# Kernel tuning notes

Hardware: AMD Instinct MI355X
Metric: run time of the kernel (lower is better)

The kernel has to match this reference:

```python
import jax, jax.numpy as jnp
import numpy as np

EPS = 1e-5

def _linear(x, w, b):
    # torch nn.Linear convention: w is [out, in]
    return jnp.einsum('...i,oi->...o', x, w) + b

def _l2_normalize(x, axis=-1):
    n = jnp.sqrt(jnp.sum(x * x, axis=axis, keepdims=True))
    return x / jnp.maximum(n, 1e-12)

def _online_softmax_scan(sim):
    # sim: [B, H, L]. Running max m_t and running sum s_t = sum_{i<=t} exp(sim_i - m_t)
    def combine(a, b):
        ma, sa = a
        mb, sb = b
        m = jnp.maximum(ma, mb)
        s = sa * jnp.exp(ma - m) + sb * jnp.exp(mb - m)
        return m, s
    m_scan, s_scan = jax.lax.associative_scan(combine, (sim, jnp.ones_like(sim)), axis=2)
    return m_scan, s_scan


def setup_inputs() -> dict:
    key = jax.random.key(0)
    ks = jax.random.split(key, 8)
    B, L, D = 2, 2048, 256
    H, h = 8, 32
    s = 1.0 / np.sqrt(D)
    inp = {
        'x': jax.random.normal(ks[0], (B, L, D), jnp.float32),
        'wq_w': jax.random.normal(ks[1], (D, D), jnp.float32) * s,
        'wq_b': jnp.zeros((D,), jnp.float32),
        'wk_w': jax.random.normal(ks[2], (D, D), jnp.float32) * s,
        'wk_b': jnp.zeros((D,), jnp.float32),
        'wv_w': jax.random.normal(ks[3], (D, D), jnp.float32) * s,
        'wv_b': jnp.zeros((D,), jnp.float32),
        'wo_w': jax.random.normal(ks[4], (D, D), jnp.float32) * s,
        'wo_b': jnp.zeros((D,), jnp.float32),
        'wg_w': jax.random.normal(ks[5], (1, h * h), jnp.float32) * (1.0 / np.sqrt(h * h)),
        'wg_b': jnp.zeros((1,), jnp.float32),
        'kv_norm_scale': jnp.ones((1, H, 1, h, h), jnp.float32),
        'qk_norm_scale': jnp.full((1, H, 1), 1.0 / np.sqrt(h), jnp.float32),
    }
    return inp


def reference(x, wq_w, wq_b, wk_w, wk_b, wv_w, wv_b, wo_w, wo_b,
              wg_w, wg_b, kv_norm_scale, qk_norm_scale):
    B, L, D = x.shape
    H, h = kv_norm_scale.shape[1], kv_norm_scale.shape[3]

    q = _linear(x, wq_w, wq_b).reshape(B, L, H, h).transpose(0, 2, 1, 3)  # bhld
    k = _linear(x, wk_w, wk_b).reshape(B, L, H, h).transpose(0, 2, 1, 3)
    v = _linear(x, wv_w, wv_b).reshape(B, L, H, h).transpose(0, 2, 1, 3)

    sim = jnp.einsum('bhld,bhld->bhl', q, k) * qk_norm_scale  # [B,H,L]

    k = _l2_normalize(k)
    v = _l2_normalize(v)

    # outer-product KV state per position: [B,H,L,h,h]
    Z = jnp.einsum('bhld,bhle->bhlde', v, k) * kv_norm_scale

    # gating: squared ReLU of linear over flattened h*h features
    gate_inputs = Z.reshape(B, H, L, h * h)
    gates_logits = jnp.einsum('bhli,oi->bhlo', gate_inputs, wg_w) + wg_b  # [B,H,L,1]
    gates = jnp.square(jax.nn.relu(gates_logits)) + EPS
    gates = gates[..., None]  # [B,H,L,1,1]
    gated_Z = gates * Z

    # associative scans along L
    m_scan, s_scan = _online_softmax_scan(sim)        # [B,H,L]
    Z_scan = jnp.cumsum(gated_Z, axis=2)              # [B,H,L,h,h]
    g_scan = jnp.cumsum(gates, axis=2)                # [B,H,L,1,1]

    softmax_weights = (jnp.exp(sim - m_scan) / (s_scan + EPS))[..., None, None]
    gated_weights = Z_scan / (g_scan + EPS)
    attn_weights = gated_weights * (1.0 + jax.nn.silu(softmax_weights))

    ctxt = jnp.einsum('bhld,bhlde->bhle', q, attn_weights)
    ctxt = ctxt.transpose(0, 2, 1, 3).reshape(B, L, D)
    return _linear(ctxt, wo_w, wo_b)
```

## Files before the change

### kernel.cpp

```cpp
#include <hip/hip_runtime.h>
#include <math.h>

#define EPSV 1e-5f

static constexpr int Ls = 2048, Hh = 8;
static constexpr int NCH = 64, T = 32;

typedef unsigned short u16;
using frag  = __attribute__((ext_vector_type(8))) short;
using f32x4 = __attribute__((ext_vector_type(4))) float;

__device__ __forceinline__ void split_bf16(float v, u16& hi, u16& lo) {
    const unsigned u = __float_as_uint(v);
    hi = (u16)(u >> 16);
    const float hf = __uint_as_float((unsigned)hi << 16);
    lo = (u16)(__float_as_uint(v - hf) >> 16);
}

__device__ __forceinline__ unsigned pk2(u16 a, u16 b) {
    return (unsigned)a | ((unsigned)b << 16);
}

__device__ __forceinline__ void split8(const float4& a, const float4& b,
                                       uint4& hi, uint4& lo) {
    u16 h[8], l[8];
    const float f[8] = {a.x, a.y, a.z, a.w, b.x, b.y, b.z, b.w};
#pragma unroll
    for (int i = 0; i < 8; ++i) split_bf16(f[i], h[i], l[i]);
    hi = make_uint4(pk2(h[0], h[1]), pk2(h[2], h[3]), pk2(h[4], h[5]), pk2(h[6], h[7]));
    lo = make_uint4(pk2(l[0], l[1]), pk2(l[2], l[3]), pk2(l[4], l[5]), pk2(l[6], l[7]));
}

__global__ __launch_bounds__(256) void qkv_fused(
    const float* __restrict__ x,
    const float* __restrict__ wq, const float* __restrict__ wk, const float* __restrict__ wv,
    const float* __restrict__ bq, const float* __restrict__ bk, const float* __restrict__ bv,
    const float* __restrict__ wg_w, const float* __restrict__ wg_b,
    const float* __restrict__ kvs, const float* __restrict__ qks,
    float* __restrict__ qh, float* __restrict__ kh, float* __restrict__ vh,
    float* __restrict__ simG, float* __restrict__ gG,
    float* __restrict__ ZcT, float* __restrict__ mT, float* __restrict__ sT,
    float* __restrict__ gTt)
{
    constexpr int LDK = 40;
    constexpr int LDT = 68;
    __shared__ __align__(16) float smemf[3 * 64 * LDT];
    __shared__ __align__(16) float wkT[2][32 * 36];
    __shared__ float lsim[2][64], lg2[2][64];

    u16* As_hi = (u16*)smemf;
    u16* As_lo = As_hi + 2560;
    u16* Wst   = As_lo + 2560;
    float* Qt = smemf;
    float* Kt = Qt + 64 * LDT;
    float* Vt = Kt + 64 * LDT;

    const int tid = threadIdx.x;
    const int mt = blockIdx.x, nt = blockIdx.y;
    const int m0 = mt * 64, ncol0 = nt * 64;
    const int bidx = m0 >> 11, lg = m0 & (Ls - 1);
    const int wave = tid >> 6, lane = tid & 63;
    const int l15 = lane & 15, quad = lane >> 4;
    const int srow = tid >> 2, sk = (tid & 3) * 8;

    for (int i = tid; i < 2048; i += 256) {
        const int h = i >> 10, de = i & 1023;
        const int d = de >> 5, e = de & 31;
        wkT[h][e * 36 + d] = wg_w[de] * kvs[(nt * 2 + h) * 1024 + de];
    }

    const float* Wsrc[3] = {wq, wk, wv};
    f32x4 acc[3][4] = {};

    for (int k0 = 0; k0 < 256; k0 += 32) {
        const float4 a0 = *(const float4*)&x[(size_t)(m0 + srow) * 256 + k0 + sk];
        const float4 a1 = *(const float4*)&x[(size_t)(m0 + srow) * 256 + k0 + sk + 4];
        float4 w0[3], w1[3];
#pragma unroll
        for (int w = 0; w < 3; ++w) {
            w0[w] = *(const float4*)&Wsrc[w][(size_t)(ncol0 + srow) * 256 + k0 + sk];
            w1[w] = *(const float4*)&Wsrc[w][(size_t)(ncol0 + srow) * 256 + k0 + sk + 4];
        }
        __syncthreads();
        {
            uint4 hi, lo;
            split8(a0, a1, hi, lo);
            *(uint4*)&As_hi[srow * LDK + sk] = hi;
            *(uint4*)&As_lo[srow * LDK + sk] = lo;
#pragma unroll
            for (int w = 0; w < 3; ++w) {
                split8(w0[w], w1[w], hi, lo);
                *(uint4*)&Wst[w * 5120 + srow * LDK + sk] = hi;
                *(uint4*)&Wst[w * 5120 + 2560 + srow * LDK + sk] = lo;
            }
        }
        __syncthreads();

        const frag ah = *(const frag*)&As_hi[(wave * 16 + l15) * LDK + quad * 8];
        const frag al = *(const frag*)&As_lo[(wave * 16 + l15) * LDK + quad * 8];
#pragma unroll
        for (int w = 0; w < 3; ++w)
#pragma unroll
            for (int cf = 0; cf < 4; ++cf) {
                const u16* bp = &Wst[w * 5120 + (cf * 16 + l15) * LDK + quad * 8];
                const frag bh = *(const frag*)bp;
                const frag bl = *(const frag*)(bp + 2560);
                acc[w][cf] = __builtin_amdgcn_mfma_f32_16x16x32_bf16(ah, bh, acc[w][cf], 0, 0, 0);
                acc[w][cf] = __builtin_amdgcn_mfma_f32_16x16x32_bf16(ah, bl, acc[w][cf], 0, 0, 0);
                acc[w][cf] = __builtin_amdgcn_mfma_f32_16x16x32_bf16(al, bh, acc[w][cf], 0, 0, 0);
            }
    }
    __syncthreads();

    {
        float* tiles[3] = {Qt, Kt, Vt};
        const float* biases[3] = {bq, bk, bv};
#pragma unroll
        for (int w = 0; w < 3; ++w)
#pragma unroll
            for (int cf = 0; cf < 4; ++cf) {
                const int col = cf * 16 + l15;
                const float bias = biases[w][ncol0 + col];
#pragma unroll
                for (int r = 0; r < 4; ++r) {
                    const int m = wave * 16 + quad * 4 + r;
                    tiles[w][m * LDT + col] = acc[w][cf][r] + bias;
                }
            }
    }
    __syncthreads();

    if (tid < 128) {
        const int h = tid >> 6, l = tid & 63;
        const int rb = l * LDT + h * 32;
        float4 kr[8], vr[8];
        float ksum = 0.f, vsum = 0.f, qk = 0.f;
#pragma unroll
        for (int e4 = 0; e4 < 8; ++e4) {
            kr[e4] = *(const float4*)&Kt[rb + e4 * 4];
            vr[e4] = *(const float4*)&Vt[rb + e4 * 4];
            const float4 q4 = *(const float4*)&Qt[rb + e4 * 4];
            ksum += kr[e4].x * kr[e4].x + kr[e4].y * kr[e4].y + kr[e4].z * kr[e4].z + kr[e4].w * kr[e4].w;
            vsum += vr[e4].x * vr[e4].x + vr[e4].y * vr[e4].y + vr[e4].z * vr[e4].z + vr[e4].w * vr[e4].w;
            qk   += q4.x * kr[e4].x + q4.y * kr[e4].y + q4.z * kr[e4].z + q4.w * kr[e4].w;
        }
        const float kscale = 1.f / fmaxf(sqrtf(ksum), 1e-12f);
        const float vscale = 1.f / fmaxf(sqrtf(vsum), 1e-12f);
#pragma unroll
        for (int e4 = 0; e4 < 8; ++e4) {
            float4 k4 = kr[e4], v4 = vr[e4];
            k4.x *= kscale; k4.y *= kscale; k4.z *= kscale; k4.w *= kscale;
            v4.x *= vscale; v4.y *= vscale; v4.z *= vscale; v4.w *= vscale;
            *(float4*)&Kt[rb + e4 * 4] = k4;
            *(float4*)&Vt[rb + e4 * 4] = v4;
        }
        const float sim = qk * qks[nt * 2 + h];
        lsim[h][l] = sim;
        simG[(size_t)(bidx * 8 + nt * 2 + h) * Ls + lg + l] = sim;
    }
    __syncthreads();

    {
        const float* tl[3] = {Qt, Kt, Vt};
        float* gl[3] = {qh, kh, vh};
#pragma unroll
        for (int arr = 0; arr < 3; ++arr)
#pragma unroll
            for (int it = 0; it < 4; ++it) {
                const int idx = it * 1024 + tid * 4;
                const int h = idx >> 11, rem = idx & 2047;
                const int l = rem >> 5, e4 = rem & 31;
                const float4 v = *(const float4*)&tl[arr][l * LDT + h * 32 + e4];
                *(float4*)&gl[arr][(size_t)(bidx * 8 + nt * 2 + h) * 65536 +
                                   (size_t)(lg + l) * 32 + e4] = v;
            }
    }

    {
        const int task = tid >> 1, half = tid & 1;
        const int h = task >> 6, l = task & 63;
        float4 vr[8];
#pragma unroll
        for (int d4 = 0; d4 < 8; ++d4)
            vr[d4] = *(const float4*)&Vt[l * LDT + h * 32 + d4 * 4];
        float u = 0.f;
        const int e0 = half * 16;
#pragma unroll 4
        for (int e = e0; e < e0 + 16; ++e) {
            float4 s4 = make_float4(0.f, 0.f, 0.f, 0.f);
#pragma unroll
            for (int d4 = 0; d4 < 8; ++d4) {
                const float4 w4 = *(const float4*)&wkT[h][e * 36 + d4 * 4];
                s4.x = fmaf(vr[d4].x, w4.x, s4.x);
                s4.y = fmaf(vr[d4].y, w4.y, s4.y);
                s4.z = fmaf(vr[d4].z, w4.z, s4.z);
                s4.w = fmaf(vr[d4].w, w4.w, s4.w);
            }
            u = fmaf(s4.x + s4.y + s4.z + s4.w, Kt[l * LDT + h * 32 + e], u);
        }
        u += __shfl_xor(u, 1);
        if (half == 0) {
            const float r = fmaxf(u + wg_b[0], 0.f);
            const float g = r * r + EPSV;
            lg2[h][l] = g;
            gG[(size_t)(bidx * 8 + nt * 2 + h) * Ls + lg + l] = g;
        }
    }
    __syncthreads();

    {
        const int d = tid >> 3, e4m = (tid & 7) * 4;
#pragma unroll
        for (int h = 0; h < 2; ++h)
#pragma unroll
            for (int cc = 0; cc < 2; ++cc) {
                float4 z4 = make_float4(0.f, 0.f, 0.f, 0.f);
#pragma unroll 8
                for (int l = 0; l < 32; ++l) {
                    const int lr = cc * 32 + l;
                    const float gv = lg2[h][lr] * Vt[lr * LDT + h * 32 + d];
                    const float4 k4 = *(const float4*)&Kt[lr * LDT + h * 32 + e4m];
                    z4.x = fmaf(gv, k4.x, z4.x);
                    z4.y = fmaf(gv, k4.y, z4.y);
                    z4.z = fmaf(gv, k4.z, z4.z);
                    z4.w = fmaf(gv, k4.w, z4.w);
                }
                const int bhg = bidx * 8 + nt * 2 + h;
                const int cg = (lg >> 5) + cc;
                *(float4*)&ZcT[((size_t)bhg * NCH + cg) * 1024 + d * 32 + e4m] = z4;
            }
    }

    {
        const int h = wave >> 1, cc = wave & 1;
        if (lane < 32) {
            const int lr = cc * 32 + lane;
            float m = lsim[h][lr], s = 1.f, g = lg2[h][lr];
#pragma unroll
            for (int off = 16; off; off >>= 1) {
                const float mo = __shfl_xor(m, off);
                const float so = __shfl_xor(s, off);
                const float mn = fmaxf(m, mo);
                s = s * __expf(m - mn) + so * __expf(mo - mn);
                m = mn;
                g += __shfl_xor(g, off);
            }
            if (lane == 0) {
                const int bhg = bidx * 8 + nt * 2 + h;
                const int cg = (lg >> 5) + cc;
                mT[bhg * NCH + cg] = m;
                sT[bhg * NCH + cg] = s;
                gTt[bhg * NCH + cg] = g;
            }
        }
    }
}

__global__ __launch_bounds__(256) void prefix_kernel(
    float* __restrict__ Zc, float* __restrict__ mT, float* __restrict__ sT,
    float* __restrict__ gTt,
    const float* __restrict__ kvs, float* __restrict__ aW, float* __restrict__ bW,
    int* __restrict__ flagW)
{
    __shared__ float sc[64 * 64];
    const int bh = blockIdx.x, seg = blockIdx.y;
    const int tid = threadIdx.x;
    float* Zb = Zc + (size_t)bh * NCH * 1024 + seg * 64;

#pragma unroll
    for (int it = 0; it < 16; ++it) {
        const int idx = it * 256 + tid;
        const int cc = idx >> 6, e = idx & 63;
        sc[idx] = Zb[(size_t)cc * 1024 + e];
    }
    __syncthreads();
#pragma unroll
    for (int st = 1; st < 64; st <<= 1) {
        float tmp[16];
#pragma unroll
        for (int it = 0; it < 16; ++it) {
            const int idx = it * 256 + tid;
            tmp[it] = ((idx >> 6) >= st) ? sc[idx - st * 64] : 0.f;
        }
        __syncthreads();
#pragma unroll
        for (int it = 0; it < 16; ++it) sc[it * 256 + tid] += tmp[it];
        __syncthreads();
    }
#pragma unroll
    for (int it = 0; it < 16; ++it) {
        const int idx = it * 256 + tid;
        const int cc = idx >> 6, e = idx & 63;
        Zb[(size_t)cc * 1024 + e] = cc ? sc[idx - 64] : 0.f;
    }

    if (seg == 0 && tid < 64) {
        float m = mT[bh * NCH + tid], s = sT[bh * NCH + tid], g = gTt[bh * NCH + tid];
#pragma unroll
        for (int off = 1; off < 64; off <<= 1) {
            const float mo = __shfl_up(m, off);
            const float so = __shfl_up(s, off);
            const float go = __shfl_up(g, off);
            if (tid >= off) {
                const float mn = fmaxf(m, mo);
                s = s * __expf(m - mn) + so * __expf(mo - mn);
                m = mn;
                g += go;
            }
        }
        float me = __shfl_up(m, 1), se = __shfl_up(s, 1), ge = __shfl_up(g, 1);
        if (tid == 0) { me = -1e30f; se = 0.f; ge = 0.f; }
        mT[bh * NCH + tid] = me;
        sT[bh * NCH + tid] = se;
        gTt[bh * NCH + tid] = ge;
    }

    if (bh == 0 && seg == 1) {
        const int h = tid >> 5, e = tid & 31;
        const float* K = kvs + h * 1024;
        const float k00 = K[0];
        int ok = (k00 != 0.0f);
        for (int d = 0; d < 32; ++d) {
            const float lhs = K[d * 32 + e] * k00;
            const float rhs = K[d * 32] * K[e];
            const float diff = fabsf(lhs - rhs);
            if (diff > 1e-6f * fmaxf(fmaxf(fabsf(lhs), fabsf(rhs)), 1e-20f)) ok = 0;
        }
        aW[h * 32 + e] = K[e * 32];
        bW[h * 32 + e] = (k00 != 0.0f) ? K[e] / k00 : 0.f;
        const int allok = __syncthreads_and(ok);
        if (tid == 0) flagW[0] = allok;
    }
}

__global__ __launch_bounds__(256) void chunk_out_kernel(
    const float* __restrict__ qh, const float* __restrict__ knG, const float* __restrict__ vnG,
    const float* __restrict__ simG, const float* __restrict__ gG,
    const float* __restrict__ kvs,
    const float* __restrict__ ZcP, const float* __restrict__ mP,
    const float* __restrict__ sP, const float* __restrict__ gP,
    const float* __restrict__ aW, const float* __restrict__ bW,
    const int* __restrict__ flagW,
    u16* __restrict__ chi, u16* __restrict__ clo)
{
    __shared__ __align__(16) float qa[1024], knb[1024], zp[1024], sW[1024];
    __shared__ __align__(16) float vnT[32 * 36];
    __shared__ float lkvs[1024];
    __shared__ float lgS[32], lsimS[32], lwgt[32];
    const int tid = threadIdx.x;
    const int c = blockIdx.x, bh = blockIdx.y, h = bh & 7, b = bh >> 3;
    const int l = tid >> 3, e4 = (tid & 7) * 4;
    const size_t base4 = ((size_t)bh * Ls + (size_t)c * T) * 8 + tid;
    const int flag = flagW[0];

    const float4 qv4 = ((const float4*)qh)[base4];
    const float4 kn4 = ((const float4*)knG)[base4];
    const float4 vn4 = ((const float4*)vnG)[base4];
    const float4 z4  = ((const float4*)ZcP)[((size_t)bh * NCH + c) * 256 + tid];
    const float4 la4 = *(const float4*)&aW[h * 32 + e4];
    const float4 lb4 = *(const float4*)&bW[h * 32 + e4];
    if (tid < 32) {
        lgS[tid] = gG[bh * Ls + c * T + tid];
        lsimS[tid] = simG[bh * Ls + c * T + tid];
    }
    if (!flag) {
        *(float4*)&lkvs[tid * 4] = *(const float4*)&kvs[h * 1024 + tid * 4];
    }
    {
        float4 q = qv4, k = kn4;
        if (flag) {
            q.x *= la4.x; q.y *= la4.y; q.z *= la4.z; q.w *= la4.w;
            k.x *= lb4.x; k.y *= lb4.y; k.z *= lb4.z; k.w *= lb4.w;
        }
        *(float4*)&qa[l * 32 + e4] = q;
        *(float4*)&knb[l * 32 + e4] = k;
        *(float4*)&zp[tid * 4] = z4;
        vnT[(e4 + 0) * 36 + l] = vn4.x;
        vnT[(e4 + 1) * 36 + l] = vn4.y;
        vnT[(e4 + 2) * 36 + l] = vn4.z;
        vnT[(e4 + 3) * 36 + l] = vn4.w;
    }
    __syncthreads();

    if (tid < 32) {
        float m = lsimS[tid], s = 1.f, g = lgS[tid];
#pragma unroll
        for (int off = 1; off < 32; off <<= 1) {
            const float mo = __shfl_up(m, off);
            const float so = __shfl_up(s, off);
            const float go = __shfl_up(g, off);
            if (tid >= off) {
                const float mn = fmaxf(m, mo);
                s = s * __expf(m - mn) + so * __expf(mo - mn);
                m = mn;
                g += go;
            }
        }
        const float mp = mP[bh * NCH + c];
        const float sp = sP[bh * NCH + c];
        const float gp = gP[bh * NCH + c];
        const float mn = fmaxf(mp, m);
        s = sp * __expf(mp - mn) + s * __expf(m - mn);
        m = mn;
        g += gp;
        const float sw = __expf(lsimS[tid] - m) / (s + EPSV);
        const float sig = 1.f / (1.f + __expf(-sw));
        lwgt[tid] = (1.f + sw * sig) / (g + EPSV);
    }

    float4 y4 = make_float4(0.f, 0.f, 0.f, 0.f);
    if (flag) {
        float qrow[32];
#pragma unroll
        for (int d4 = 0; d4 < 8; ++d4)
            *(float4*)&qrow[d4 * 4] = *(const float4*)&qa[l * 32 + d4 * 4];
        float4 s4 = make_float4(0.f, 0.f, 0.f, 0.f);
#pragma unroll 8
        for (int d = 0; d < 32; ++d) {
            const float qd = qrow[d];
            const float4 v4 = *(const float4*)&vnT[d * 36 + e4];
            const float4 p4 = *(const float4*)&zp[d * 32 + e4];
            s4.x = fmaf(qd, v4.x, s4.x);
            s4.y = fmaf(qd, v4.y, s4.y);
            s4.z = fmaf(qd, v4.z, s4.z);
            s4.w = fmaf(qd, v4.w, s4.w);
            y4.x = fmaf(qd, p4.x, y4.x);
            y4.y = fmaf(qd, p4.y, y4.y);
            y4.z = fmaf(qd, p4.z, y4.z);
            y4.w = fmaf(qd, p4.w, y4.w);
        }
        y4.x *= lb4.x; y4.y *= lb4.y; y4.z *= lb4.z; y4.w *= lb4.w;
        const float4 lg4 = *(const float4*)&lgS[e4];
        float4 sm;
        sm.x = (e4 + 0 <= l) ? lg4.x * s4.x : 0.f;
        sm.y = (e4 + 1 <= l) ? lg4.y * s4.y : 0.f;
        sm.z = (e4 + 2 <= l) ? lg4.z * s4.z : 0.f;
        sm.w = (e4 + 3 <= l) ? lg4.w * s4.w : 0.f;
        *(float4*)&sW[l * 32 + e4] = sm;
        __syncthreads();
        float srow[32];
#pragma unroll
        for (int j4 = 0; j4 < 8; ++j4)
            *(float4*)&srow[j4 * 4] = *(const float4*)&sW[l * 32 + j4 * 4];
#pragma unroll 8
        for (int j = 0; j < 32; ++j) {
            const float sj = srow[j];
            const float4 k4 = *(const float4*)&knb[j * 32 + e4];
            y4.x = fmaf(sj, k4.x, y4.x);
            y4.y = fmaf(sj, k4.y, y4.y);
            y4.z = fmaf(sj, k4.z, y4.z);
            y4.w = fmaf(sj, k4.w, y4.w);
        }
    } else {
        __syncthreads();
        float* yp = &y4.x;
#pragma unroll
        for (int i = 0; i < 4; ++i) {
            const int e = e4 + i;
            float qe[32];
#pragma unroll
            for (int d = 0; d < 32; ++d)
                qe[d] = qa[l * 32 + d] * lkvs[d * 32 + e];
            float y = 0.f;
#pragma unroll
            for (int d = 0; d < 32; ++d)
                y = fmaf(qe[d], zp[d * 32 + e], y);
            for (int j = 0; j < 32; ++j) {
                float s = 0.f;
#pragma unroll
                for (int d = 0; d < 32; ++d)
                    s = fmaf(qe[d], vnT[d * 36 + j], s);
                if (j <= l) y = fmaf(lgS[j] * s, knb[j * 32 + e], y);
            }
            yp[i] = y;
        }
    }
    const float w = lwgt[l];
    ushort4 hi4, lo4;
    split_bf16(y4.x * w, hi4.x, lo4.x);
    split_bf16(y4.y * w, hi4.y, lo4.y);
    split_bf16(y4.z * w, hi4.z, lo4.z);
    split_bf16(y4.w * w, hi4.w, lo4.w);
    const size_t oidx = ((size_t)(b * Ls + c * T + l)) * 256 + h * 32 + e4;
    *(ushort4*)&chi[oidx] = hi4;
    *(ushort4*)&clo[oidx] = lo4;
}

__global__ __launch_bounds__(256) void out_gemm(
    const u16* __restrict__ Ahi, const u16* __restrict__ Alo,
    const float* __restrict__ wo, const float* __restrict__ bo,
    float* __restrict__ out)
{
    constexpr int LDK = 40;
    __shared__ __align__(16) u16 As_hi[64 * LDK];
    __shared__ __align__(16) u16 As_lo[64 * LDK];
    __shared__ __align__(16) u16 Ws_hi[64 * LDK];
    __shared__ __align__(16) u16 Ws_lo[64 * LDK];

    const int tid = threadIdx.x;
    const int mt = blockIdx.x, nt = blockIdx.y;
    const int m0 = mt * 64, ncol0 = nt * 64;
    const int wave = tid >> 6, lane = tid & 63;
    const int l15 = lane & 15, quad = lane >> 4;
    const int srow = tid >> 2, sk = (tid & 3) * 8;

    f32x4 acc[4] = {};

    for (int k0 = 0; k0 < 256; k0 += 32) {
        const uint4 ah = *(const uint4*)&Ahi[(size_t)(m0 + srow) * 256 + k0 + sk];
        const uint4 al = *(const uint4*)&Alo[(size_t)(m0 + srow) * 256 + k0 + sk];
        const float4 w0 = *(const float4*)&wo[(size_t)(ncol0 + srow) * 256 + k0 + sk];
        const float4 w1 = *(const float4*)&wo[(size_t)(ncol0 + srow) * 256 + k0 + sk + 4];
        __syncthreads();
        uint4 whi, wlo;
        split8(w0, w1, whi, wlo);
        *(uint4*)&As_hi[srow * LDK + sk] = ah;
        *(uint4*)&As_lo[srow * LDK + sk] = al;
        *(uint4*)&Ws_hi[srow * LDK + sk] = whi;
        *(uint4*)&Ws_lo[srow * LDK + sk] = wlo;
        __syncthreads();

        const frag fah = *(const frag*)&As_hi[(wave * 16 + l15) * LDK + quad * 8];
        const frag fal = *(const frag*)&As_lo[(wave * 16 + l15) * LDK + quad * 8];
#pragma unroll
        for (int cf = 0; cf < 4; ++cf) {
            const frag fbh = *(const frag*)&Ws_hi[(cf * 16 + l15) * LDK + quad * 8];
            const frag fbl = *(const frag*)&Ws_lo[(cf * 16 + l15) * LDK + quad * 8];
            acc[cf] = __builtin_amdgcn_mfma_f32_16x16x32_bf16(fah, fbh, acc[cf], 0, 0, 0);
            acc[cf] = __builtin_amdgcn_mfma_f32_16x16x32_bf16(fah, fbl, acc[cf], 0, 0, 0);
            acc[cf] = __builtin_amdgcn_mfma_f32_16x16x32_bf16(fal, fbh, acc[cf], 0, 0, 0);
        }
    }

#pragma unroll
    for (int cf = 0; cf < 4; ++cf) {
        const int o = ncol0 + cf * 16 + l15;
        const float bias = bo[o];
#pragma unroll
        for (int r = 0; r < 4; ++r) {
            const int rm = m0 + wave * 16 + quad * 4 + r;
            out[(size_t)rm * 256 + o] = acc[cf][r] + bias;
        }
    }
}

extern "C" void kernel_launch(void* const* d_in, const int* in_sizes, int n_in,
                              void* d_out, int out_size, void* d_ws, size_t ws_size,
                              hipStream_t stream) {
    const float* x    = (const float*)d_in[0];
    const float* wq_w = (const float*)d_in[1];
    const float* wq_b = (const float*)d_in[2];
    const float* wk_w = (const float*)d_in[3];
    const float* wk_b = (const float*)d_in[4];
    const float* wv_w = (const float*)d_in[5];
    const float* wv_b = (const float*)d_in[6];
    const float* wo_w = (const float*)d_in[7];
    const float* wo_b = (const float*)d_in[8];
    const float* wg_w = (const float*)d_in[9];
    const float* wg_b = (const float*)d_in[10];
    const float* kvs  = (const float*)d_in[11];
    const float* qks  = (const float*)d_in[12];
    float* out = (float*)d_out;

    u16* chi = (u16*)d_ws;
    u16* clo = chi + 1048576;
    float* qh   = (float*)(clo + 1048576);
    float* kh   = qh + 1048576;
    float* vh   = kh + 1048576;
    float* ZcT  = vh + 1048576;
    float* simG = ZcT + 1048576;
    float* gG   = simG + 32768;
    float* mT   = gG + 32768;
    float* sT   = mT + 1024;
    float* gTt  = sT + 1024;
    float* aW   = gTt + 1024;
    float* bW   = aW + 256;
    int* flagW  = (int*)(bW + 256);

    qkv_fused<<<dim3(64, 4), 256, 0, stream>>>(
        x, wq_w, wk_w, wv_w, wq_b, wk_b, wv_b, wg_w, wg_b, kvs, qks,
        qh, kh, vh, simG, gG, ZcT, mT, sT, gTt);
    prefix_kernel<<<dim3(16, 16), 256, 0, stream>>>(
        ZcT, mT, sT, gTt, kvs, aW, bW, flagW);
    chunk_out_kernel<<<dim3(NCH, 16), 256, 0, stream>>>(
        qh, kh, vh, simG, gG, kvs, ZcT, mT, sT, gTt, aW, bW, flagW, chi, clo);
    out_gemm<<<dim3(64, 4), 256, 0, stream>>>(
        chi, clo, wo_w, wo_b, out);
}
```

Measured before the change: 157.6 us.

## Merge four kernels into one cooperative persistent kernel with grid syncs

Folds the QKV projection, prefix scan, chunk output and output GEMM kernels into a single mega_kernel that is launched cooperatively with 256 blocks and separates phases with grid-wide syncs. If cooperative launch is unavailable or fails, it falls back to four per-phase launches. The goal is to remove the launch gaps between kernels. The phase-0 GEMM is also re-tiled so each wave owns 16 output columns and walks all four row tiles, reusing each B fragment. Risks: the middle phases have to be remapped onto 256 blocks, grid syncs cost time, and a register-heavy body may limit occupancy.

```diff
diff --git a/kernel.cpp b/kernel.cpp
--- a/kernel.cpp
+++ b/kernel.cpp
@@ -1,7 +1,10 @@
 #include <hip/hip_runtime.h>
+#include <hip/hip_cooperative_groups.h>
 #include <math.h>
 
 #define EPSV 1e-5f
+
+namespace cg = cooperative_groups;
 
 static constexpr int Ls = 2048, Hh = 8;
 static constexpr int NCH = 64, T = 32;
@@ -31,515 +34,518 @@
     lo = make_uint4(pk2(l[0], l[1]), pk2(l[2], l[3]), pk2(l[4], l[5]), pk2(l[6], l[7]));
 }
 
-__global__ __launch_bounds__(256) void qkv_fused(
-    const float* __restrict__ x,
-    const float* __restrict__ wq, const float* __restrict__ wk, const float* __restrict__ wv,
-    const float* __restrict__ bq, const float* __restrict__ bk, const float* __restrict__ bv,
-    const float* __restrict__ wg_w, const float* __restrict__ wg_b,
-    const float* __restrict__ kvs, const float* __restrict__ qks,
-    float* __restrict__ qh, float* __restrict__ kh, float* __restrict__ vh,
-    float* __restrict__ simG, float* __restrict__ gG,
-    float* __restrict__ ZcT, float* __restrict__ mT, float* __restrict__ sT,
-    float* __restrict__ gTt)
-{
-    constexpr int LDK = 40;
-    constexpr int LDT = 68;
-    __shared__ __align__(16) float smemf[3 * 64 * LDT];
-    __shared__ __align__(16) float wkT[2][32 * 36];
-    __shared__ float lsim[2][64], lg2[2][64];
-
-    u16* As_hi = (u16*)smemf;
-    u16* As_lo = As_hi + 2560;
-    u16* Wst   = As_lo + 2560;
-    float* Qt = smemf;
-    float* Kt = Qt + 64 * LDT;
-    float* Vt = Kt + 64 * LDT;
+struct Params {
+    const float *x, *wq, *wk, *wv, *bq, *bk, *bv, *wo, *bo, *wg_w, *wg_b, *kvs, *qks;
+    float *qh, *kh, *vh, *simG, *gG, *ZcT, *mT, *sT, *gTt, *aW, *bW;
+    int* flagW;
+    u16 *chi, *clo;
+    float* out;
+};
+
+__global__ __launch_bounds__(256) void mega_kernel(Params p, int phase) {
+    __shared__ __align__(16) float smem[15616];
 
     const int tid = threadIdx.x;
-    const int mt = blockIdx.x, nt = blockIdx.y;
-    const int m0 = mt * 64, ncol0 = nt * 64;
-    const int bidx = m0 >> 11, lg = m0 & (Ls - 1);
+    const int bid = blockIdx.x;
     const int wave = tid >> 6, lane = tid & 63;
     const int l15 = lane & 15, quad = lane >> 4;
-    const int srow = tid >> 2, sk = (tid & 3) * 8;
-
-    for (int i = tid; i < 2048; i += 256) {
-        const int h = i >> 10, de = i & 1023;
-        const int d = de >> 5, e = de & 31;
-        wkT[h][e * 36 + d] = wg_w[de] * kvs[(nt * 2 + h) * 1024 + de];
-    }
-
-    const float* Wsrc[3] = {wq, wk, wv};
-    f32x4 acc[3][4] = {};
-
-    for (int k0 = 0; k0 < 256; k0 += 32) {
-        const float4 a0 = *(const float4*)&x[(size_t)(m0 + srow) * 256 + k0 + sk];
-        const float4 a1 = *(const float4*)&x[(size_t)(m0 + srow) * 256 + k0 + sk + 4];
-        float4 w0[3], w1[3];
-#pragma unroll
-        for (int w = 0; w < 3; ++w) {
-            w0[w] = *(const float4*)&Wsrc[w][(size_t)(ncol0 + srow) * 256 + k0 + sk];
-            w1[w] = *(const float4*)&Wsrc[w][(size_t)(ncol0 + srow) * 256 + k0 + sk + 4];
-        }
-        __syncthreads();
-        {
-            uint4 hi, lo;
-            split8(a0, a1, hi, lo);
-            *(uint4*)&As_hi[srow * LDK + sk] = hi;
-            *(uint4*)&As_lo[srow * LDK + sk] = lo;
+
+    if (phase < 0 || phase == 0) {
+        constexpr int LDK = 40;
+        constexpr int LDT = 68;
+        u16* As_hi = (u16*)smem;
+        u16* As_lo = As_hi + 2560;
+        u16* Wst   = As_lo + 2560;
+        float* Qt = smem;
+        float* Kt = Qt + 64 * LDT;
+        float* Vt = Kt + 64 * LDT;
+        float* wkT  = smem + 13056;
+        float* lsim = smem + 15360;
+        float* lg2  = smem + 15488;
+
+        const int mt = bid & 63, nt = bid >> 6;
+        const int m0 = mt * 64, ncol0 = nt * 64;
+        const int bidx = m0 >> 11, lg = m0 & (Ls - 1);
+        const int srow = tid >> 2, sk = (tid & 3) * 8;
+
+        for (int i = tid; i < 2048; i += 256) {
+            const int h = i >> 10, de = i & 1023;
+            const int d = de >> 5, e = de & 31;
+            wkT[h * 1152 + e * 36 + d] = p.wg_w[de] * p.kvs[(nt * 2 + h) * 1024 + de];
+        }
+
+        const float* Wsrc[3] = {p.wq, p.wk, p.wv};
+        f32x4 acc[3][4] = {};
+
+        for (int k0 = 0; k0 < 256; k0 += 32) {
+            const float4 a0 = *(const float4*)&p.x[(size_t)(m0 + srow) * 256 + k0 + sk];
+            const float4 a1 = *(const float4*)&p.x[(size_t)(m0 + srow) * 256 + k0 + sk + 4];
+            float4 w0[3], w1[3];
 #pragma unroll
             for (int w = 0; w < 3; ++w) {
-                split8(w0[w], w1[w], hi, lo);
-                *(uint4*)&Wst[w * 5120 + srow * LDK + sk] = hi;
-                *(uint4*)&Wst[w * 5120 + 2560 + srow * LDK + sk] = lo;
-            }
-        }
-        __syncthreads();
-
-        const frag ah = *(const frag*)&As_hi[(wave * 16 + l15) * LDK + quad * 8];
-        const frag al = *(const frag*)&As_lo[(wave * 16 + l15) * LDK + quad * 8];
-#pragma unroll
-        for (int w = 0; w < 3; ++w)
-#pragma unroll
-            for (int cf = 0; cf < 4; ++cf) {
-                const u16* bp = &Wst[w * 5120 + (cf * 16 + l15) * LDK + quad * 8];
+                w0[w] = *(const float4*)&Wsrc[w][(size_t)(ncol0 + srow) * 256 + k0 + sk];
+                w1[w] = *(const float4*)&Wsrc[w][(size_t)(ncol0 + srow) * 256 + k0 + sk + 4];
+            }
+            __syncthreads();
+            {
+                uint4 hi, lo;
+                split8(a0, a1, hi, lo);
+                *(uint4*)&As_hi[srow * LDK + sk] = hi;
+                *(uint4*)&As_lo[srow * LDK + sk] = lo;
+#pragma unroll
+                for (int w = 0; w < 3; ++w) {
+                    split8(w0[w], w1[w], hi, lo);
+                    *(uint4*)&Wst[w * 5120 + srow * LDK + sk] = hi;
+                    *(uint4*)&Wst[w * 5120 + 2560 + srow * LDK + sk] = lo;
+                }
+            }
+            __syncthreads();
+
+            frag ah[4], al[4];
+#pragma unroll
+            for (int tm = 0; tm < 4; ++tm) {
+                const int r = tm * 16 + l15;
+                ah[tm] = *(const frag*)&As_hi[r * LDK + quad * 8];
+                al[tm] = *(const frag*)&As_lo[r * LDK + quad * 8];
+            }
+#pragma unroll
+            for (int w = 0; w < 3; ++w) {
+                const u16* bp = &Wst[w * 5120 + (wave * 16 + l15) * LDK + quad * 8];
                 const frag bh = *(const frag*)bp;
                 const frag bl = *(const frag*)(bp + 2560);
-                acc[w][cf] = __builtin_amdgcn_mfma_f32_16x16x32_bf16(ah, bh, acc[w][cf], 0, 0, 0);
-                acc[w][cf] = __builtin_amdgcn_mfma_f32_16x16x32_bf16(ah, bl, acc[w][cf], 0, 0, 0);
-                acc[w][cf] = __builtin_amdgcn_mfma_f32_16x16x32_bf16(al, bh, acc[w][cf], 0, 0, 0);
-            }
+#pragma unroll
+                for (int tm = 0; tm < 4; ++tm) {
+                    acc[w][tm] = __builtin_amdgcn_mfma_f32_16x16x32_bf16(ah[tm], bh, acc[w][tm], 0, 0, 0);
+                    acc[w][tm] = __builtin_amdgcn_mfma_f32_16x16x32_bf16(ah[tm], bl, acc[w][tm], 0, 0, 0);
+                    acc[w][tm] = __builtin_amdgcn_mfma_f32_16x16x32_bf16(al[tm], bh, acc[w][tm], 0, 0, 0);
+                }
+            }
+        }
+        __syncthreads();
+
+        {
+            float* tiles[3] = {Qt, Kt, Vt};
+            const float* biases[3] = {p.bq, p.bk, p.bv};
+#pragma unroll
+            for (int w = 0; w < 3; ++w) {
+                const int col = wave * 16 + l15;
+                const float bias = biases[w][ncol0 + col];
+#pragma unroll
+                for (int tm = 0; tm < 4; ++tm)
+#pragma unroll
+                    for (int r = 0; r < 4; ++r) {
+                        const int m = tm * 16 + quad * 4 + r;
+                        tiles[w][m * LDT + col] = acc[w][tm][r] + bias;
+                    }
+            }
+        }
+        __syncthreads();
+
+        if (tid < 128) {
+            const int h = tid >> 6, l = tid & 63;
+            const int rb = l * LDT + h * 32;
+            float4 kr[8], vr[8];
+            float ksum = 0.f, vsum = 0.f, qk = 0.f;
+#pragma unroll
+            for (int e4 = 0; e4 < 8; ++e4) {
+                kr[e4] = *(const float4*)&Kt[rb + e4 * 4];
+                vr[e4] = *(const float4*)&Vt[rb + e4 * 4];
+                const float4 q4 = *(const float4*)&Qt[rb + e4 * 4];
+                ksum += kr[e4].x * kr[e4].x + kr[e4].y * kr[e4].y + kr[e4].z * kr[e4].z + kr[e4].w * kr[e4].w;
+                vsum += vr[e4].x * vr[e4].x + vr[e4].y * vr[e4].y + vr[e4].z * vr[e4].z + vr[e4].w * vr[e4].w;
+                qk   += q4.x * kr[e4].x + q4.y * kr[e4].y + q4.z * kr[e4].z + q4.w * kr[e4].w;
+            }
+            const float kscale = 1.f / fmaxf(sqrtf(ksum), 1e-12f);
+            const float vscale = 1.f / fmaxf(sqrtf(vsum), 1e-12f);
+#pragma unroll
+            for (int e4 = 0; e4 < 8; ++e4) {
+                float4 k4 = kr[e4], v4 = vr[e4];
+                k4.x *= kscale; k4.y *= kscale; k4.z *= kscale; k4.w *= kscale;
+                v4.x *= vscale; v4.y *= vscale; v4.z *= vscale; v4.w *= vscale;
+                *(float4*)&Kt[rb + e4 * 4] = k4;
+                *(float4*)&Vt[rb + e4 * 4] = v4;
+            }
+            const float sim = qk * p.qks[nt * 2 + h];
+            lsim[h * 64 + l] = sim;
+            p.simG[(size_t)(bidx * 8 + nt * 2 + h) * Ls + lg + l] = sim;
+        }
+        __syncthreads();
+
+        {
+            const float* tl[3] = {Qt, Kt, Vt};
+            float* gl[3] = {p.qh, p.kh, p.vh};
+#pragma unroll
+            for (int arr = 0; arr < 3; ++arr)
+#pragma unroll
+                for (int it = 0; it < 4; ++it) {
+                    const int idx = it * 1024 + tid * 4;
+                    const int h = idx >> 11, rem = idx & 2047;
+                    const int l = rem >> 5, e4 = rem & 31;
+                    const float4 v = *(const float4*)&tl[arr][l * LDT + h * 32 + e4];
+                    *(float4*)&gl[arr][(size_t)(bidx * 8 + nt * 2 + h) * 65536 +
+                                       (size_t)(lg + l) * 32 + e4] = v;
+                }
+        }
+
+        {
+            const int task = tid >> 1, half = tid & 1;
+            const int h = task >> 6, l = task & 63;
+            float4 vr[8];
+#pragma unroll
+            for (int d4 = 0; d4 < 8; ++d4)
+                vr[d4] = *(const float4*)&Vt[l * LDT + h * 32 + d4 * 4];
+            float u = 0.f;
+            const int e0 = half * 16;
+#pragma unroll 4
+            for (int e = e0; e < e0 + 16; ++e) {
+                float4 s4 = make_float4(0.f, 0.f, 0.f, 0.f);
+#pragma unroll
+                for (int d4 = 0; d4 < 8; ++d4) {
+                    const float4 w4 = *(const float4*)&wkT[h * 1152 + e * 36 + d4 * 4];
+                    s4.x = fmaf(vr[d4].x, w4.x, s4.x);
+                    s4.y = fmaf(vr[d4].y, w4.y, s4.y);
+                    s4.z = fmaf(vr[d4].z, w4.z, s4.z);
+                    s4.w = fmaf(vr[d4].w, w4.w, s4.w);
+                }
+                u = fmaf(s4.x + s4.y + s4.z + s4.w, Kt[l * LDT + h * 32 + e], u);
+            }
+            u += __shfl_xor(u, 1);
+            if (half == 0) {
+                const float r = fmaxf(u + p.wg_b[0], 0.f);
+                const float g = r * r + EPSV;
+                lg2[h * 64 + l] = g;
+                p.gG[(size_t)(bidx * 8 + nt * 2 + h) * Ls + lg + l] = g;
+            }
+        }
+        __syncthreads();
+
+        {
+            const int d = tid >> 3, e4m = (tid & 7) * 4;
+#pragma unroll
+            for (int h = 0; h < 2; ++h)
+#pragma unroll
+                for (int cc = 0; cc < 2; ++cc) {
+                    float4 z4 = make_float4(0.f, 0.f, 0.f, 0.f);
+#pragma unroll 8
+                    for (int l = 0; l < 32; ++l) {
+                        const int lr = cc * 32 + l;
+                        const float gv = lg2[h * 64 + lr] * Vt[lr * LDT + h * 32 + d];
+                        const float4 k4 = *(const float4*)&Kt[lr * LDT + h * 32 + e4m];
+                        z4.x = fmaf(gv, k4.x, z4.x);
+                        z4.y = fmaf(gv, k4.y, z4.y);
+                        z4.z = fmaf(gv, k4.z, z4.z);
+                        z4.w = fmaf(gv, k4.w, z4.w);
+                    }
+                    const int bhg = bidx * 8 + nt * 2 + h;
+                    const int cg = (lg >> 5) + cc;
+                    *(float4*)&p.ZcT[((size_t)bhg * NCH + cg) * 1024 + d * 32 + e4m] = z4;
+                }
+        }
+
+        {
+            const int h = wave >> 1, cc = wave & 1;
+            if (lane < 32) {
+                const int lr = cc * 32 + lane;
+                float m = lsim[h * 64 + lr], s = 1.f, g = lg2[h * 64 + lr];
+#pragma unroll
+                for (int off = 16; off; off >>= 1) {
+                    const float mo = __shfl_xor(m, off);
+                    const float so = __shfl_xor(s, off);
+                    const float mn = fmaxf(m, mo);
+                    s = s * __expf(m - mn) + so * __expf(mo - mn);
+                    m = mn;
+                    g += __shfl_xor(g, off);
+                }
+                if (lane == 0) {
+                    const int bhg = bidx * 8 + nt * 2 + h;
+                    const int cg = (lg >> 5) + cc;
+                    p.mT[bhg * NCH + cg] = m;
+                    p.sT[bhg * NCH + cg] = s;
+                    p.gTt[bhg * NCH + cg] = g;
+                }
+            }
+        }
     }
-    __syncthreads();
-
-    {
-        float* tiles[3] = {Qt, Kt, Vt};
-        const float* biases[3] = {bq, bk, bv};
-#pragma unroll
-        for (int w = 0; w < 3; ++w)
-#pragma unroll
-            for (int cf = 0; cf < 4; ++cf) {
-                const int col = cf * 16 + l15;
-                const float bias = biases[w][ncol0 + col];
-#pragma unroll
-                for (int r = 0; r < 4; ++r) {
-                    const int m = wave * 16 + quad * 4 + r;
-                    tiles[w][m * LDT + col] = acc[w][cf][r] + bias;
-                }
-            }
-    }
-    __syncthreads();
-
-    if (tid < 128) {
-        const int h = tid >> 6, l = tid & 63;
-        const int rb = l * LDT + h * 32;
-        float4 kr[8], vr[8];
-        float ksum = 0.f, vsum = 0.f, qk = 0.f;
-#pragma unroll
-        for (int e4 = 0; e4 < 8; ++e4) {
-            kr[e4] = *(const float4*)&Kt[rb + e4 * 4];
-            vr[e4] = *(const float4*)&Vt[rb + e4 * 4];
-            const float4 q4 = *(const float4*)&Qt[rb + e4 * 4];
-            ksum += kr[e4].x * kr[e4].x + kr[e4].y * kr[e4].y + kr[e4].z * kr[e4].z + kr[e4].w * kr[e4].w;
-            vsum += vr[e4].x * vr[e4].x + vr[e4].y * vr[e4].y + vr[e4].z * vr[e4].z + vr[e4].w * vr[e4].w;
-            qk   += q4.x * kr[e4].x + q4.y * kr[e4].y + q4.z * kr[e4].z + q4.w * kr[e4].w;
-        }
-        const float kscale = 1.f / fmaxf(sqrtf(ksum), 1e-12f);
-        const float vscale = 1.f / fmaxf(sqrtf(vsum), 1e-12f);
-#pragma unroll
-        for (int e4 = 0; e4 < 8; ++e4) {
-            float4 k4 = kr[e4], v4 = vr[e4];
-            k4.x *= kscale; k4.y *= kscale; k4.z *= kscale; k4.w *= kscale;
-            v4.x *= vscale; v4.y *= vscale; v4.z *= vscale; v4.w *= vscale;
-            *(float4*)&Kt[rb + e4 * 4] = k4;
-            *(float4*)&Vt[rb + e4 * 4] = v4;
-        }
-        const float sim = qk * qks[nt * 2 + h];
-        lsim[h][l] = sim;
-        simG[(size_t)(bidx * 8 + nt * 2 + h) * Ls + lg + l] = sim;
-    }
-    __syncthreads();
-
-    {
-        const float* tl[3] = {Qt, Kt, Vt};
-        float* gl[3] = {qh, kh, vh};
-#pragma unroll
-        for (int arr = 0; arr < 3; ++arr)
-#pragma unroll
-            for (int it = 0; it < 4; ++it) {
-                const int idx = it * 1024 + tid * 4;
-                const int h = idx >> 11, rem = idx & 2047;
-                const int l = rem >> 5, e4 = rem & 31;
-                const float4 v = *(const float4*)&tl[arr][l * LDT + h * 32 + e4];
-                *(float4*)&gl[arr][(size_t)(bidx * 8 + nt * 2 + h) * 65536 +
-                                   (size_t)(lg + l) * 32 + e4] = v;
-            }
-    }
-
-    {
-        const int task = tid >> 1, half = tid & 1;
-        const int h = task >> 6, l = task & 63;
-        float4 vr[8];
-#pragma unroll
-        for (int d4 = 0; d4 < 8; ++d4)
-            vr[d4] = *(const float4*)&Vt[l * LDT + h * 32 + d4 * 4];
-        float u = 0.f;
-        const int e0 = half * 16;
-#pragma unroll 4
-        for (int e = e0; e < e0 + 16; ++e) {
-            float4 s4 = make_float4(0.f, 0.f, 0.f, 0.f);
-#pragma unroll
-            for (int d4 = 0; d4 < 8; ++d4) {
-                const float4 w4 = *(const float4*)&wkT[h][e * 36 + d4 * 4];
-                s4.x = fmaf(vr[d4].x, w4.x, s4.x);
-                s4.y = fmaf(vr[d4].y, w4.y, s4.y);
-                s4.z = fmaf(vr[d4].z, w4.z, s4.z);
-                s4.w = fmaf(vr[d4].w, w4.w, s4.w);
-            }
-            u = fmaf(s4.x + s4.y + s4.z + s4.w, Kt[l * LDT + h * 32 + e], u);
-        }
-        u += __shfl_xor(u, 1);
-        if (half == 0) {
-            const float r = fmaxf(u + wg_b[0], 0.f);
-            const float g = r * r + EPSV;
-            lg2[h][l] = g;
-            gG[(size_t)(bidx * 8 + nt * 2 + h) * Ls + lg + l] = g;
-        }
-    }
-    __syncthreads();
-
-    {
-        const int d = tid >> 3, e4m = (tid & 7) * 4;
-#pragma unroll
-        for (int h = 0; h < 2; ++h)
-#pragma unroll
-            for (int cc = 0; cc < 2; ++cc) {
-                float4 z4 = make_float4(0.f, 0.f, 0.f, 0.f);
-#pragma unroll 8
-                for (int l = 0; l < 32; ++l) {
-                    const int lr = cc * 32 + l;
-                    const float gv = lg2[h][lr] * Vt[lr * LDT + h * 32 + d];
-                    const float4 k4 = *(const float4*)&Kt[lr * LDT + h * 32 + e4m];
-                    z4.x = fmaf(gv, k4.x, z4.x);
-                    z4.y = fmaf(gv, k4.y, z4.y);
-                    z4.z = fmaf(gv, k4.z, z4.z);
-                    z4.w = fmaf(gv, k4.w, z4.w);
-                }
-                const int bhg = bidx * 8 + nt * 2 + h;
-                const int cg = (lg >> 5) + cc;
-                *(float4*)&ZcT[((size_t)bhg * NCH + cg) * 1024 + d * 32 + e4m] = z4;
-            }
-    }
-
-    {
-        const int h = wave >> 1, cc = wave & 1;
-        if (lane < 32) {
-            const int lr = cc * 32 + lane;
-            float m = lsim[h][lr], s = 1.f, g = lg2[h][lr];
-#pragma unroll
-            for (int off = 16; off; off >>= 1) {
-                const float mo = __shfl_xor(m, off);
-                const float so = __shfl_xor(s, off);
-                const float mn = fmaxf(m, mo);
-                s = s * __expf(m - mn) + so * __expf(mo - mn);
-                m = mn;
-                g += __shfl_xor(g, off);
-            }
-            if (lane == 0) {
-                const int bhg = bidx * 8 + nt * 2 + h;
-                const int cg = (lg >> 5) + cc;
-                mT[bhg * NCH + cg] = m;
-                sT[bhg * NCH + cg] = s;
-                gTt[bhg * NCH + cg] = g;
-            }
-        }
-    }
-}
-
-__global__ __launch_bounds__(256) void prefix_kernel(
-    float* __restrict__ Zc, float* __restrict__ mT, float* __restrict__ sT,
-    float* __restrict__ gTt,
-    const float* __restrict__ kvs, float* __restrict__ aW, float* __restrict__ bW,
-    int* __restrict__ flagW)
-{
-    __shared__ float sc[64 * 64];
-    const int bh = blockIdx.x, seg = blockIdx.y;
-    const int tid = threadIdx.x;
-    float* Zb = Zc + (size_t)bh * NCH * 1024 + seg * 64;
-
-#pragma unroll
-    for (int it = 0; it < 16; ++it) {
-        const int idx = it * 256 + tid;
-        const int cc = idx >> 6, e = idx & 63;
-        sc[idx] = Zb[(size_t)cc * 1024 + e];
-    }
-    __syncthreads();
-#pragma unroll
-    for (int st = 1; st < 64; st <<= 1) {
-        float tmp[16];
+
+    if (phase < 0) cg::this_grid().sync();
+
+    if (phase < 0 || phase == 1) {
+        float* sc = smem;
+        const int bh = bid >> 4, seg = bid & 15;
+        float* Zb = p.ZcT + (size_t)bh * NCH * 1024 + seg * 64;
+
 #pragma unroll
         for (int it = 0; it < 16; ++it) {
             const int idx = it * 256 + tid;
-            tmp[it] = ((idx >> 6) >= st) ? sc[idx - st * 64] : 0.f;
+            const int cc = idx >> 6, e = idx & 63;
+            sc[idx] = Zb[(size_t)cc * 1024 + e];
         }
         __syncthreads();
 #pragma unroll
-        for (int it = 0; it < 16; ++it) sc[it * 256 + tid] += tmp[it];
-        __syncthreads();
+        for (int st = 1; st < 64; st <<= 1) {
+            float tmp[16];
+#pragma unroll
+            for (int it = 0; it < 16; ++it) {
+                const int idx = it * 256 + tid;
+                tmp[it] = ((idx >> 6) >= st) ? sc[idx - st * 64] : 0.f;
+            }
+            __syncthreads();
+#pragma unroll
+            for (int it = 0; it < 16; ++it) sc[it * 256 + tid] += tmp[it];
+            __syncthreads();
+        }
+#pragma unroll
+        for (int it = 0; it < 16; ++it) {
+            const int idx = it * 256 + tid;
+            const int cc = idx >> 6, e = idx & 63;
+            Zb[(size_t)cc * 1024 + e] = cc ? sc[idx - 64] : 0.f;
+        }
+
+        if (seg == 0 && tid < 64) {
+            float m = p.mT[bh * NCH + tid], s = p.sT[bh * NCH + tid], g = p.gTt[bh * NCH + tid];
+#pragma unroll
+            for (int off = 1; off < 64; off <<= 1) {
+                const float mo = __shfl_up(m, off);
+                const float so = __shfl_up(s, off);
+                const float go = __shfl_up(g, off);
+                if (tid >= off) {
+                    const float mn = fmaxf(m, mo);
+                    s = s * __expf(m - mn) + so * __expf(mo - mn);
+                    m = mn;
+                    g += go;
+                }
+            }
+            float me = __shfl_up(m, 1), se = __shfl_up(s, 1), ge = __shfl_up(g, 1);
+            if (tid == 0) { me = -1e30f; se = 0.f; ge = 0.f; }
+            p.mT[bh * NCH + tid] = me;
+            p.sT[bh * NCH + tid] = se;
+            p.gTt[bh * NCH + tid] = ge;
+        }
+
+        if (bid == 1) {
+            const int h = tid >> 5, e = tid & 31;
+            const float* K = p.kvs + h * 1024;
+            const float k00 = K[0];
+            int ok = (k00 != 0.0f);
+            for (int d = 0; d < 32; ++d) {
+                const float lhs = K[d * 32 + e] * k00;
+                const float rhs = K[d * 32] * K[e];
+                const float diff = fabsf(lhs - rhs);
+                if (diff > 1e-6f * fmaxf(fmaxf(fabsf(lhs), fabsf(rhs)), 1e-20f)) ok = 0;
+            }
+            p.aW[h * 32 + e] = K[e * 32];
+            p.bW[h * 32 + e] = (k00 != 0.0f) ? K[e] / k00 : 0.f;
+            const int allok = __syncthreads_and(ok);
+            if (tid == 0) p.flagW[0] = allok;
+        }
     }
-#pragma unroll
-    for (int it = 0; it < 16; ++it) {
-        const int idx = it * 256 + tid;
-        const int cc = idx >> 6, e = idx & 63;
-        Zb[(size_t)cc * 1024 + e] = cc ? sc[idx - 64] : 0.f;
+
+    if (phase < 0) cg::this_grid().sync();
+
+    if (phase < 0 || phase == 2) {
+        float* qa   = smem;
+        float* knb  = smem + 1024;
+        float* zp   = smem + 2048;
+        float* sW   = smem + 3072;
+        float* vnT  = smem + 4096;
+        float* lkvs = smem + 5248;
+        float* lgS  = smem + 6272;
+        float* lsimS= smem + 6304;
+        float* lwgt = smem + 6336;
+
+        const int bh = bid & 15, h = bh & 7, b = bh >> 3;
+        const int l = tid >> 3, e4 = (tid & 7) * 4;
+        const int flag = p.flagW[0];
+
+        for (int i = 0; i < 4; ++i) {
+            const int c = (bid >> 4) * 4 + i;
+            __syncthreads();
+
+            const size_t base4 = ((size_t)bh * Ls + (size_t)c * T) * 8 + tid;
+            const float4 qv4 = ((const float4*)p.qh)[base4];
+            const float4 kn4 = ((const float4*)p.kh)[base4];
+            const float4 vn4 = ((const float4*)p.vh)[base4];
+            const float4 z4  = ((const float4*)p.ZcT)[((size_t)bh * NCH + c) * 256 + tid];
+            const float4 la4 = *(const float4*)&p.aW[h * 32 + e4];
+            const float4 lb4 = *(const float4*)&p.bW[h * 32 + e4];
+            if (tid < 32) {
+                lgS[tid] = p.gG[bh * Ls + c * T + tid];
+                lsimS[tid] = p.simG[bh * Ls + c * T + tid];
+            }
+            if (!flag) {
+                *(float4*)&lkvs[tid * 4] = *(const float4*)&p.kvs[h * 1024 + tid * 4];
+            }
+            {
+                float4 q = qv4, k = kn4;
+                if (flag) {
+                    q.x *= la4.x; q.y *= la4.y; q.z *= la4.z; q.w *= la4.w;
+                    k.x *= lb4.x; k.y *= lb4.y; k.z *= lb4.z; k.w *= lb4.w;
+                }
+                *(float4*)&qa[l * 32 + e4] = q;
+                *(float4*)&knb[l * 32 + e4] = k;
+                *(float4*)&zp[tid * 4] = z4;
+                vnT[(e4 + 0) * 36 + l] = vn4.x;
+                vnT[(e4 + 1) * 36 + l] = vn4.y;
+                vnT[(e4 + 2) * 36 + l] = vn4.z;
+                vnT[(e4 + 3) * 36 + l] = vn4.w;
+            }
+            __syncthreads();
+
+            if (tid < 32) {
+                float m = lsimS[tid], s = 1.f, g = lgS[tid];
+#pragma unroll
+                for (int off = 1; off < 32; off <<= 1) {
+                    const float mo = __shfl_up(m, off);
+                    const float so = __shfl_up(s, off);
+                    const float go = __shfl_up(g, off);
+                    if (tid >= off) {
+                        const float mn = fmaxf(m, mo);
+                        s = s * __expf(m - mn) + so * __expf(mo - mn);
+                        m = mn;
+                        g += go;
+                    }
+                }
+                const float mp = p.mT[bh * NCH + c];
+                const float sp = p.sT[bh * NCH + c];
+                const float gp = p.gTt[bh * NCH + c];
+                const float mn = fmaxf(mp, m);
+                s = sp * __expf(mp - mn) + s * __expf(m - mn);
+                m = mn;
+                g += gp;
+                const float sw = __expf(lsimS[tid] - m) / (s + EPSV);
+                const float sig = 1.f / (1.f + __expf(-sw));
+                lwgt[tid] = (1.f + sw * sig) / (g + EPSV);
+            }
+
+            float4 y4 = make_float4(0.f, 0.f, 0.f, 0.f);
+            if (flag) {
+                float qrow[32];
+#pragma unroll
+                for (int d4 = 0; d4 < 8; ++d4)
+                    *(float4*)&qrow[d4 * 4] = *(const float4*)&qa[l * 32 + d4 * 4];
+                float4 s4 = make_float4(0.f, 0.f, 0.f, 0.f);
+#pragma unroll 8
+                for (int d = 0; d < 32; ++d) {
+                    const float qd = qrow[d];
+                    const float4 v4 = *(const float4*)&vnT[d * 36 + e4];
+                    const float4 p4 = *(const float4*)&zp[d * 32 + e4];
+                    s4.x = fmaf(qd, v4.x, s4.x);
+                    s4.y = fmaf(qd, v4.y, s4.y);
+                    s4.z = fmaf(qd, v4.z, s4.z);
+                    s4.w = fmaf(qd, v4.w, s4.w);
+                    y4.x = fmaf(qd, p4.x, y4.x);
+                    y4.y = fmaf(qd, p4.y, y4.y);
+                    y4.z = fmaf(qd, p4.z, y4.z);
+                    y4.w = fmaf(qd, p4.w, y4.w);
+                }
+                y4.x *= lb4.x; y4.y *= lb4.y; y4.z *= lb4.z; y4.w *= lb4.w;
+                const float4 lg4 = *(const float4*)&lgS[e4];
+                float4 sm;
+                sm.x = (e4 + 0 <= l) ? lg4.x * s4.x : 0.f;
+                sm.y = (e4 + 1 <= l) ? lg4.y * s4.y : 0.f;
+                sm.z = (e4 + 2 <= l) ? lg4.z * s4.z : 0.f;
+                sm.w = (e4 + 3 <= l) ? lg4.w * s4.w : 0.f;
+                *(float4*)&sW[l * 32 + e4] = sm;
+                __syncthreads();
+                float srow[32];
+#pragma unroll
+                for (int j4 = 0; j4 < 8; ++j4)
+                    *(float4*)&srow[j4 * 4] = *(const float4*)&sW[l * 32 + j4 * 4];
+#pragma unroll 8
+                for (int j = 0; j < 32; ++j) {
+                    const float sj = srow[j];
+                    const float4 k4 = *(const float4*)&knb[j * 32 + e4];
+                    y4.x = fmaf(sj, k4.x, y4.x);
+                    y4.y = fmaf(sj, k4.y, y4.y);
+                    y4.z = fmaf(sj, k4.z, y4.z);
+                    y4.w = fmaf(sj, k4.w, y4.w);
+                }
+            } else {
+                __syncthreads();
+                float* yp = &y4.x;
+#pragma unroll
+                for (int ii = 0; ii < 4; ++ii) {
+                    const int e = e4 + ii;
+                    float qe[32];
+#pragma unroll
+                    for (int d = 0; d < 32; ++d)
+                        qe[d] = qa[l * 32 + d] * lkvs[d * 32 + e];
+                    float y = 0.f;
+#pragma unroll
+                    for (int d = 0; d < 32; ++d)
+                        y = fmaf(qe[d], zp[d * 32 + e], y);
+                    for (int j = 0; j < 32; ++j) {
+                        float s = 0.f;
+#pragma unroll
+                        for (int d = 0; d < 32; ++d)
+                            s = fmaf(qe[d], vnT[d * 36 + j], s);
+                        if (j <= l) y = fmaf(lgS[j] * s, knb[j * 32 + e], y);
+                    }
+                    yp[ii] = y;
+                }
+            }
+            const float w = lwgt[l];
+            ushort4 hi4, lo4;
+            split_bf16(y4.x * w, hi4.x, lo4.x);
+            split_bf16(y4.y * w, hi4.y, lo4.y);
+            split_bf16(y4.z * w, hi4.z, lo4.z);
+            split_bf16(y4.w * w, hi4.w, lo4.w);
+            const size_t oidx = ((size_t)(b * Ls + c * T + l)) * 256 + h * 32 + e4;
+            *(ushort4*)&p.chi[oidx] = hi4;
+            *(ushort4*)&p.clo[oidx] = lo4;
+        }
     }
 
-    if (seg == 0 && tid < 64) {
-        float m = mT[bh * NCH + tid], s = sT[bh * NCH + tid], g = gTt[bh * NCH + tid];
-#pragma unroll
-        for (int off = 1; off < 64; off <<= 1) {
-            const float mo = __shfl_up(m, off);
-            const float so = __shfl_up(s, off);
-            const float go = __shfl_up(g, off);
-            if (tid >= off) {
-                const float mn = fmaxf(m, mo);
-                s = s * __expf(m - mn) + so * __expf(mo - mn);
-                m = mn;
-                g += go;
-            }
-        }
-        float me = __shfl_up(m, 1), se = __shfl_up(s, 1), ge = __shfl_up(g, 1);
-        if (tid == 0) { me = -1e30f; se = 0.f; ge = 0.f; }
-        mT[bh * NCH + tid] = me;
-        sT[bh * NCH + tid] = se;
-        gTt[bh * NCH + tid] = ge;
-    }
-
-    if (bh == 0 && seg == 1) {
-        const int h = tid >> 5, e = tid & 31;
-        const float* K = kvs + h * 1024;
-        const float k00 = K[0];
-        int ok = (k00 != 0.0f);
-        for (int d = 0; d < 32; ++d) {
-            const float lhs = K[d * 32 + e] * k00;
-            const float rhs = K[d * 32] * K[e];
-            const float diff = fabsf(lhs - rhs);
-            if (diff > 1e-6f * fmaxf(fmaxf(fabsf(lhs), fabsf(rhs)), 1e-20f)) ok = 0;
-        }
-        aW[h * 32 + e] = K[e * 32];
-        bW[h * 32 + e] = (k00 != 0.0f) ? K[e] / k00 : 0.f;
-        const int allok = __syncthreads_and(ok);
-        if (tid == 0) flagW[0] = allok;
-    }
-}
-
-__global__ __launch_bounds__(256) void chunk_out_kernel(
-    const float* __restrict__ qh, const float* __restrict__ knG, const float* __restrict__ vnG,
-    const float* __restrict__ simG, const float* __restrict__ gG,
-    const float* __restrict__ kvs,
-    const float* __restrict__ ZcP, const float* __restrict__ mP,
-    const float* __restrict__ sP, const float* __restrict__ gP,
-    const float* __restrict__ aW, const float* __restrict__ bW,
-    const int* __restrict__ flagW,
-    u16* __restrict__ chi, u16* __restrict__ clo)
-{
-    __shared__ __align__(16) float qa[1024], knb[1024], zp[1024], sW[1024];
-    __shared__ __align__(16) float vnT[32 * 36];
-    __shared__ float lkvs[1024];
-    __shared__ float lgS[32], lsimS[32], lwgt[32];
-    const int tid = threadIdx.x;
-    const int c = blockIdx.x, bh = blockIdx.y, h = bh & 7, b = bh >> 3;
-    const int l = tid >> 3, e4 = (tid & 7) * 4;
-    const size_t base4 = ((size_t)bh * Ls + (size_t)c * T) * 8 + tid;
-    const int flag = flagW[0];
-
-    const float4 qv4 = ((const float4*)qh)[base4];
-    const float4 kn4 = ((const float4*)knG)[base4];
-    const float4 vn4 = ((const float4*)vnG)[base4];
-    const float4 z4  = ((const float4*)ZcP)[((size_t)bh * NCH + c) * 256 + tid];
-    const float4 la4 = *(const float4*)&aW[h * 32 + e4];
-    const float4 lb4 = *(const float4*)&bW[h * 32 + e4];
-    if (tid < 32) {
-        lgS[tid] = gG[bh * Ls + c * T + tid];
-        lsimS[tid] = simG[bh * Ls + c * T + tid];
-    }
-    if (!flag) {
-        *(float4*)&lkvs[tid * 4] = *(const float4*)&kvs[h * 1024 + tid * 4];
-    }
-    {
-        float4 q = qv4, k = kn4;
-        if (flag) {
-            q.x *= la4.x; q.y *= la4.y; q.z *= la4.z; q.w *= la4.w;
-            k.x *= lb4.x; k.y *= lb4.y; k.z *= lb4.z; k.w *= lb4.w;
-        }
-        *(float4*)&qa[l * 32 + e4] = q;
-        *(float4*)&knb[l * 32 + e4] = k;
-        *(float4*)&zp[tid * 4] = z4;
-        vnT[(e4 + 0) * 36 + l] = vn4.x;
-        vnT[(e4 + 1) * 36 + l] = vn4.y;
-        vnT[(e4 + 2) * 36 + l] = vn4.z;
-        vnT[(e4 + 3) * 36 + l] = vn4.w;
-    }
-    __syncthreads();
-
-    if (tid < 32) {
-        float m = lsimS[tid], s = 1.f, g = lgS[tid];
-#pragma unroll
-        for (int off = 1; off < 32; off <<= 1) {
-            const float mo = __shfl_up(m, off);
-            const float so = __shfl_up(s, off);
-            const float go = __shfl_up(g, off);
-            if (tid >= off) {
-                const float mn = fmaxf(m, mo);
-                s = s * __expf(m - mn) + so * __expf(mo - mn);
-                m = mn;
-                g += go;
-            }
-        }
-        const float mp = mP[bh * NCH + c];
-        const float sp = sP[bh * NCH + c];
-        const float gp = gP[bh * NCH + c];
-        const float mn = fmaxf(mp, m);
-        s = sp * __expf(mp - mn) + s * __expf(m - mn);
-        m = mn;
-        g += gp;
-        const float sw = __expf(lsimS[tid] - m) / (s + EPSV);
-        const float sig = 1.f / (1.f + __expf(-sw));
-        lwgt[tid] = (1.f + sw * sig) / (g + EPSV);
-    }
-
-    float4 y4 = make_float4(0.f, 0.f, 0.f, 0.f);
-    if (flag) {
-        float qrow[32];
-#pragma unroll
-        for (int d4 = 0; d4 < 8; ++d4)
-            *(float4*)&qrow[d4 * 4] = *(const float4*)&qa[l * 32 + d4 * 4];
-        float4 s4 = make_float4(0.f, 0.f, 0.f, 0.f);
-#pragma unroll 8
-        for (int d = 0; d < 32; ++d) {
-            const float qd = qrow[d];
-            const float4 v4 = *(const float4*)&vnT[d * 36 + e4];
-            const float4 p4 = *(const float4*)&zp[d * 32 + e4];
-            s4.x = fmaf(qd, v4.x, s4.x);
-            s4.y = fmaf(qd, v4.y, s4.y);
-            s4.z = fmaf(qd, v4.z, s4.z);
-            s4.w = fmaf(qd, v4.w, s4.w);
-            y4.x = fmaf(qd, p4.x, y4.x);
-            y4.y = fmaf(qd, p4.y, y4.y);
-            y4.z = fmaf(qd, p4.z, y4.z);
-            y4.w = fmaf(qd, p4.w, y4.w);
-        }
-        y4.x *= lb4.x; y4.y *= lb4.y; y4.z *= lb4.z; y4.w *= lb4.w;
-        const float4 lg4 = *(const float4*)&lgS[e4];
-        float4 sm;
-        sm.x = (e4 + 0 <= l) ? lg4.x * s4.x : 0.f;
-        sm.y = (e4 + 1 <= l) ? lg4.y * s4.y : 0.f;
-        sm.z = (e4 + 2 <= l) ? lg4.z * s4.z : 0.f;
-        sm.w = (e4 + 3 <= l) ? lg4.w * s4.w : 0.f;
-        *(float4*)&sW[l * 32 + e4] = sm;
-        __syncthreads();
-        float srow[32];
-#pragma unroll
-        for (int j4 = 0; j4 < 8; ++j4)
-            *(float4*)&srow[j4 * 4] = *(const float4*)&sW[l * 32 + j4 * 4];
-#pragma unroll 8
-        for (int j = 0; j < 32; ++j) {
-            const float sj = srow[j];
-            const float4 k4 = *(const float4*)&knb[j * 32 + e4];
-            y4.x = fmaf(sj, k4.x, y4.x);
-            y4.y = fmaf(sj, k4.y, y4.y);
-            y4.z = fmaf(sj, k4.z, y4.z);
-            y4.w = fmaf(sj, k4.w, y4.w);
-        }
-    } else {
-        __syncthreads();
-        float* yp = &y4.x;
-#pragma unroll
-        for (int i = 0; i < 4; ++i) {
-            const int e = e4 + i;
-            float qe[32];
-#pragma unroll
-            for (int d = 0; d < 32; ++d)
-                qe[d] = qa[l * 32 + d] * lkvs[d * 32 + e];
-            float y = 0.f;
-#pragma unroll
-            for (int d = 0; d < 32; ++d)
-                y = fmaf(qe[d], zp[d * 32 + e], y);
-            for (int j = 0; j < 32; ++j) {
-                float s = 0.f;
-#pragma unroll
-                for (int d = 0; d < 32; ++d)
-                    s = fmaf(qe[d], vnT[d * 36 + j], s);
-                if (j <= l) y = fmaf(lgS[j] * s, knb[j * 32 + e], y);
-            }
-            yp[i] = y;
-        }
-    }
-    const float w = lwgt[l];
-    ushort4 hi4, lo4;
-    split_bf16(y4.x * w, hi4.x, lo4.x);
-    split_bf16(y4.y * w, hi4.y, lo4.y);
-    split_bf16(y4.z * w, hi4.z, lo4.z);
-    split_bf16(y4.w * w, hi4.w, lo4.w);
-    const size_t oidx = ((size_t)(b * Ls + c * T + l)) * 256 + h * 32 + e4;
-    *(ushort4*)&chi[oidx] = hi4;
-    *(ushort4*)&clo[oidx] = lo4;
-}
-
-__global__ __launch_bounds__(256) void out_gemm(
-    const u16* __restrict__ Ahi, const u16* __restrict__ Alo,
-    const float* __restrict__ wo, const float* __restrict__ bo,
-    float* __restrict__ out)
-{
-    constexpr int LDK = 40;
-    __shared__ __align__(16) u16 As_hi[64 * LDK];
-    __shared__ __align__(16) u16 As_lo[64 * LDK];
-    __shared__ __align__(16) u16 Ws_hi[64 * LDK];
-    __shared__ __align__(16) u16 Ws_lo[64 * LDK];
-
-    const int tid = threadIdx.x;
-    const int mt = blockIdx.x, nt = blockIdx.y;
-    const int m0 = mt * 64, ncol0 = nt * 64;
-    const int wave = tid >> 6, lane = tid & 63;
-    const int l15 = lane & 15, quad = lane >> 4;
-    const int srow = tid >> 2, sk = (tid & 3) * 8;
-
-    f32x4 acc[4] = {};
-
-    for (int k0 = 0; k0 < 256; k0 += 32) {
-        const uint4 ah = *(const uint4*)&Ahi[(size_t)(m0 + srow) * 256 + k0 + sk];
-        const uint4 al = *(const uint4*)&Alo[(size_t)(m0 + srow) * 256 + k0 + sk];
-        const float4 w0 = *(const float4*)&wo[(size_t)(ncol0 + srow) * 256 + k0 + sk];
-        const float4 w1 = *(const float4*)&wo[(size_t)(ncol0 + srow) * 256 + k0 + sk + 4];
-        __syncthreads();
-        uint4 whi, wlo;
-        split8(w0, w1, whi, wlo);
-        *(uint4*)&As_hi[srow * LDK + sk] = ah;
-        *(uint4*)&As_lo[srow * LDK + sk] = al;
-        *(uint4*)&Ws_hi[srow * LDK + sk] = whi;
-        *(uint4*)&Ws_lo[srow * LDK + sk] = wlo;
-        __syncthreads();
-
-        const frag fah = *(const frag*)&As_hi[(wave * 16 + l15) * LDK + quad * 8];
-        const frag fal = *(const frag*)&As_lo[(wave * 16 + l15) * LDK + quad * 8];
+    if (phase < 0) cg::this_grid().sync();
+
+    if (phase < 0 || phase == 3) {
+        constexpr int LDK = 40;
+        u16* As_hi = (u16*)smem;
+        u16* As_lo = As_hi + 2560;
+        u16* Ws_hi = As_lo + 2560;
+        u16* Ws_lo = Ws_hi + 2560;
+
+        const int mt = bid & 63, nt = bid >> 6;
+        const int m0 = mt * 64, ncol0 = nt * 64;
+        const int srow = tid >> 2, sk = (tid & 3) * 8;
+
+        f32x4 acc[4] = {};
+
+        for (int k0 = 0; k0 < 256; k0 += 32) {
+            const uint4 ah = *(const uint4*)&p.chi[(size_t)(m0 + srow) * 256 + k0 + sk];
+            const uint4 al = *(const uint4*)&p.clo[(size_t)(m0 + srow) * 256 + k0 + sk];
+            const float4 w0 = *(const float4*)&p.wo[(size_t)(ncol0 + srow) * 256 + k0 + sk];
+            const float4 w1 = *(const float4*)&p.wo[(size_t)(ncol0 + srow) * 256 + k0 + sk + 4];
+            __syncthreads();
+            uint4 whi, wlo;
+            split8(w0, w1, whi, wlo);
+            *(uint4*)&As_hi[srow * LDK + sk] = ah;
+            *(uint4*)&As_lo[srow * LDK + sk] = al;
+            *(uint4*)&Ws_hi[srow * LDK + sk] = whi;
+            *(uint4*)&Ws_lo[srow * LDK + sk] = wlo;
+            __syncthreads();
+
+            const frag fah = *(const frag*)&As_hi[(wave * 16 + l15) * LDK + quad * 8];
+            const frag fal = *(const frag*)&As_lo[(wave * 16 + l15) * LDK + quad * 8];
+#pragma unroll
+            for (int cf = 0; cf < 4; ++cf) {
+                const frag fbh = *(const frag*)&Ws_hi[(cf * 16 + l15) * LDK + quad * 8];
+                const frag fbl = *(const frag*)&Ws_lo[(cf * 16 + l15) * LDK + quad * 8];
+                acc[cf] = __builtin_amdgcn_mfma_f32_16x16x32_bf16(fah, fbh, acc[cf], 0, 0, 0);
+                acc[cf] = __builtin_amdgcn_mfma_f32_16x16x32_bf16(fah, fbl, acc[cf], 0, 0, 0);
+                acc[cf] = __builtin_amdgcn_mfma_f32_16x16x32_bf16(fal, fbh, acc[cf], 0, 0, 0);
+            }
+        }
+
 #pragma unroll
         for (int cf = 0; cf < 4; ++cf) {
-            const frag fbh = *(const frag*)&Ws_hi[(cf * 16 + l15) * LDK + quad * 8];
-            const frag fbl = *(const frag*)&Ws_lo[(cf * 16 + l15) * LDK + quad * 8];
-            acc[cf] = __builtin_amdgcn_mfma_f32_16x16x32_bf16(fah, fbh, acc[cf], 0, 0, 0);
-            acc[cf] = __builtin_amdgcn_mfma_f32_16x16x32_bf16(fah, fbl, acc[cf], 0, 0, 0);
-            acc[cf] = __builtin_amdgcn_mfma_f32_16x16x32_bf16(fal, fbh, acc[cf], 0, 0, 0);
-        }
-    }
-
-#pragma unroll
-    for (int cf = 0; cf < 4; ++cf) {
-        const int o = ncol0 + cf * 16 + l15;
-        const float bias = bo[o];
-#pragma unroll
-        for (int r = 0; r < 4; ++r) {
-            const int rm = m0 + wave * 16 + quad * 4 + r;
-            out[(size_t)rm * 256 + o] = acc[cf][r] + bias;
+            const int o = ncol0 + cf * 16 + l15;
+            const float bias = p.bo[o];
+#pragma unroll
+            for (int r = 0; r < 4; ++r) {
+                const int rm = m0 + wave * 16 + quad * 4 + r;
+                p.out[(size_t)rm * 256 + o] = acc[cf][r] + bias;
+            }
         }
     }
 }
@@ -547,43 +553,52 @@
 extern "C" void kernel_launch(void* const* d_in, const int* in_sizes, int n_in,
                               void* d_out, int out_size, void* d_ws, size_t ws_size,
                               hipStream_t stream) {
-    const float* x    = (const float*)d_in[0];
-    const float* wq_w = (const float*)d_in[1];
-    const float* wq_b = (const float*)d_in[2];
-    const float* wk_w = (const float*)d_in[3];
-    const float* wk_b = (const float*)d_in[4];
-    const float* wv_w = (const float*)d_in[5];
-    const float* wv_b = (const float*)d_in[6];
-    const float* wo_w = (const float*)d_in[7];
-    const float* wo_b = (const float*)d_in[8];
-    const float* wg_w = (const float*)d_in[9];
-    const float* wg_b = (const float*)d_in[10];
-    const float* kvs  = (const float*)d_in[11];
-    const float* qks  = (const float*)d_in[12];
-    float* out = (float*)d_out;
+    Params p;
+    p.x    = (const float*)d_in[0];
+    p.wq   = (const float*)d_in[1];
+    p.bq   = (const float*)d_in[2];
+    p.wk   = (const float*)d_in[3];
+    p.bk   = (const float*)d_in[4];
+    p.wv   = (const float*)d_in[5];
+    p.bv   = (const float*)d_in[6];
+    p.wo   = (const float*)d_in[7];
+    p.bo   = (const float*)d_in[8];
+    p.wg_w = (const float*)d_in[9];
+    p.wg_b = (const float*)d_in[10];
+    p.kvs  = (const float*)d_in[11];
+    p.qks  = (const float*)d_in[12];
+    p.out  = (float*)d_out;
 
     u16* chi = (u16*)d_ws;
     u16* clo = chi + 1048576;
     float* qh   = (float*)(clo + 1048576);
-    float* kh   = qh + 1048576;
-    float* vh   = kh + 1048576;
-    float* ZcT  = vh + 1048576;
-    float* simG = ZcT + 1048576;
-    float* gG   = simG + 32768;
-    float* mT   = gG + 32768;
-    float* sT   = mT + 1024;
-    float* gTt  = sT + 1024;
-    float* aW   = gTt + 1024;
-    float* bW   = aW + 256;
-    int* flagW  = (int*)(bW + 256);
-
-    qkv_fused<<<dim3(64, 4), 256, 0, stream>>>(
-        x, wq_w, wk_w, wv_w, wq_b, wk_b, wv_b, wg_w, wg_b, kvs, qks,
-        qh, kh, vh, simG, gG, ZcT, mT, sT, gTt);
-    prefix_kernel<<<dim3(16, 16), 256, 0, stream>>>(
-        ZcT, mT, sT, gTt, kvs, aW, bW, flagW);
-    chunk_out_kernel<<<dim3(NCH, 16), 256, 0, stream>>>(
-        qh, kh, vh, simG, gG, kvs, ZcT, mT, sT, gTt, aW, bW, flagW, chi, clo);
-    out_gemm<<<dim3(64, 4), 256, 0, stream>>>(
-        chi, clo, wo_w, wo_b, out);
+    p.chi = chi; p.clo = clo;
+    p.qh  = qh;
+    p.kh  = qh + 1048576;
+    p.vh  = p.kh + 1048576;
+    p.ZcT = p.vh + 1048576;
+    p.simG= p.ZcT + 1048576;
+    p.gG  = p.simG + 32768;
+    p.mT  = p.gG + 32768;
+    p.sT  = p.mT + 1024;
+    p.gTt = p.sT + 1024;
+    p.aW  = p.gTt + 1024;
+    p.bW  = p.aW + 256;
+    p.flagW = (int*)(p.bW + 256);
+
+    int dev = 0, coop = 0;
+    hipGetDevice(&dev);
+    hipDeviceGetAttribute(&coop, hipDeviceAttributeCooperativeLaunch, dev);
+
+    hipError_t err = hipErrorUnknown;
+    if (coop) {
+        int ph = -1;
+        void* args[] = { &p, &ph };
+        err = hipLaunchCooperativeKernel((const void*)mega_kernel,
+                                         dim3(256), dim3(256), args, 0, stream);
+    }
+    if (err != hipSuccess) {
+        for (int ph = 0; ph < 4; ++ph)
+            mega_kernel<<<256, 256, 0, stream>>>(p, ph);
+    }
 }
```

Result: slower. 248.3 us (+57.6%).
